# Kernel tuning notes

Measured on AMD Instinct MI355X. Metric: run time of the kernel, lower is better.

Reference implementation:

```python
import jax, jax.numpy as jnp
import numpy as np

B, C, E, H = 8, 2048, 1024, 128


def setup_inputs() -> dict:
    key = jax.random.key(0)
    k1, k2, k3, k4 = jax.random.split(key, 4)
    x = jax.random.normal(k1, (B, C, E), dtype=jnp.float32)
    # store projection weights as (E, H) so projection is x @ W
    Wq = jax.random.normal(k2, (E, H), dtype=jnp.float32) * (E ** -0.5)
    Wk = jax.random.normal(k3, (E, H), dtype=jnp.float32) * (E ** -0.5)
    Wv = jax.random.normal(k4, (E, H), dtype=jnp.float32) * (E ** -0.5)
    return {"x": x, "Wq": Wq, "Wk": Wk, "Wv": Wv}


def reference(x, Wq, Wk, Wv):
    # x: (B, C, E) -> out: (B, C, H)
    _, c, e = x.shape
    q = x @ Wq  # (B, C, H)
    k = x @ Wk  # (B, C, H)
    v = x @ Wv  # (B, C, H)
    # NOTE: original scales by embed_size**0.5, not head_size**0.5
    scale = jnp.asarray(e, x.dtype) ** 0.5
    w = jnp.einsum('bqh,bkh->bqk', q, k) / scale  # (B, C, C)
    causal = jnp.tril(jnp.ones((c, c), dtype=bool))
    w = jnp.where(causal, w, -jnp.inf)
    w = jax.nn.softmax(w, axis=-1)
    # dropout_rate = 0.0 -> identity (eval mode)
    out = w @ v  # (B, C, H)
    return out
```

## Files before the change

### kernel.cpp

```cpp
#include <hip/hip_runtime.h>
#include <hip/hip_bf16.h>
#include <stdint.h>

#define B_ 8
#define C_ 2048
#define E_ 1024
#define H_ 128
#define M_ (B_*C_)
#define SLOTS_B 144

typedef __attribute__((ext_vector_type(8))) short bf16x8;
typedef __attribute__((ext_vector_type(4))) float f32x4;

__device__ __forceinline__ unsigned short f2bf(float f) {
    union { float f; unsigned int u; } v; v.f = f;
    unsigned int u = v.u;
    u += 0x7fff + ((u >> 16) & 1);
    return (unsigned short)(u >> 16);
}
__device__ __forceinline__ float bf2f(unsigned short u) {
    union { unsigned int i; float f; } v; v.i = ((unsigned int)u) << 16; return v.f;
}

#define GLOAD_LDS16(g, l) \
    __builtin_amdgcn_global_load_lds((const __attribute__((address_space(1))) void*)(g), \
                                     (__attribute__((address_space(3))) void*)(l), 16, 0, 0)

__global__ __launch_bounds__(256) void wt2_kernel(const float* __restrict__ Wq,
                                                  const float* __restrict__ Wk,
                                                  const float* __restrict__ Wv,
                                                  unsigned short* __restrict__ WT2) {
    int z = blockIdx.y;
    const float* W = (z == 0) ? Wq : (z == 1) ? Wk : Wv;
    unsigned short* o = WT2 + (size_t)z * H_ * E_;
    int gid = blockIdx.x * 256 + threadIdx.x;
    int g = gid >> 7, h = gid & 127;
    unsigned short t[8];
#pragma unroll
    for (int j = 0; j < 8; ++j)
        t[j] = f2bf(W[(size_t)(g * 8 + j) * H_ + h]);
    *(bf16x8*)&o[(size_t)(g * 128 + h) * 8] = *(const bf16x8*)t;
}

#define MF(a, b, c) __builtin_amdgcn_mfma_f32_16x16x32_bf16((a), (b), (c), 0, 0, 0)

#define ALOAD(S, T) { const float* xs_ = xrow + (T) * 64; \
    a##S##_0 = *(const float4*)xs_;  a##S##_1 = *(const float4*)(xs_ + 4); }

#define AWRITE(S, BUF) { \
    unsigned short t_[8] = {f2bf(a##S##_0.x), f2bf(a##S##_0.y), f2bf(a##S##_0.z), f2bf(a##S##_0.w), \
                            f2bf(a##S##_1.x), f2bf(a##S##_1.y), f2bf(a##S##_1.z), f2bf(a##S##_1.w)}; \
    *(bf16x8*)&As[BUF][arow][(ag ^ (arow & 7)) * 8] = *(const bf16x8*)t_; }

#define COMPUTE(BUF, T) { \
    bf16x8 bw[3][2][2]; \
    _Pragma("unroll") for (int w_ = 0; w_ < 3; ++w_) \
    _Pragma("unroll") for (int ks_ = 0; ks_ < 2; ++ks_) \
    _Pragma("unroll") for (int ni_ = 0; ni_ < 2; ++ni_) \
        bw[w_][ni_][ks_] = *(const bf16x8*)&WT2[(size_t)w_ * H_ * E_ + \
            (size_t)(((T) * 8 + ks_ * 4 + lq) * 128 + wcol + ni_ * 16 + lrow) * 8]; \
    bf16x8 af[2][2]; \
    _Pragma("unroll") for (int mi_ = 0; mi_ < 2; ++mi_) \
    _Pragma("unroll") for (int ks_ = 0; ks_ < 2; ++ks_) { \
        int ra_ = mi_ * 16 + lrow; \
        af[mi_][ks_] = *(const bf16x8*)&As[BUF][ra_][((ks_ * 4 + lq) ^ (ra_ & 7)) * 8]; \
    } \
    _Pragma("unroll") for (int ks_ = 0; ks_ < 2; ++ks_) \
    _Pragma("unroll") for (int w_ = 0; w_ < 3; ++w_) \
    _Pragma("unroll") for (int ni_ = 0; ni_ < 2; ++ni_) \
    _Pragma("unroll") for (int mi_ = 0; mi_ < 2; ++mi_) \
        acc[w_][mi_][ni_] = MF(af[mi_][ks_], bw[w_][ni_][ks_], acc[w_][mi_][ni_]); }

#define EVEN_STEP(K) { \
    __syncthreads(); \
    if ((K) + 1 <= 15) AWRITE(B, 1);                \
    if ((K) + 2 <= 15) ALOAD(A, (K) + 2); \
    COMPUTE(0, K); }

#define ODD_STEP(K) { \
    __syncthreads(); \
    if ((K) + 1 <= 15) AWRITE(A, 0);                \
    if ((K) + 2 <= 15) ALOAD(B, (K) + 2); \
    COMPUTE(1, K); }

__global__ __launch_bounds__(256) void proj_kernel(const float* __restrict__ x,
                                                   const unsigned short* __restrict__ WT2,
                                                   unsigned short* __restrict__ QKV) {
    __shared__ __align__(16) unsigned short As[2][32][64];

    const int tid = threadIdx.x;
    const int wid = tid >> 6, lane = tid & 63;
    const int lrow = lane & 15, lq = lane >> 4;
    const int wcol = wid * 32;
    const int row0 = blockIdx.x * 32;

    const int arow = tid >> 3;
    const int ag = tid & 7;
    const float* xrow = x + (size_t)(row0 + arow) * E_ + ag * 8;

    f32x4 acc[3][2][2];
#pragma unroll
    for (int w = 0; w < 3; ++w)
#pragma unroll
        for (int mi = 0; mi < 2; ++mi)
#pragma unroll
            for (int ni = 0; ni < 2; ++ni) acc[w][mi][ni] = (f32x4){0.f, 0.f, 0.f, 0.f};

    float4 aA_0, aA_1, aB_0, aB_1;

    ALOAD(A, 0);
    AWRITE(A, 0);
    ALOAD(B, 1);

    EVEN_STEP(0)  ODD_STEP(1)  EVEN_STEP(2)  ODD_STEP(3)
    EVEN_STEP(4)  ODD_STEP(5)  EVEN_STEP(6)  ODD_STEP(7)
    EVEN_STEP(8)  ODD_STEP(9)  EVEN_STEP(10) ODD_STEP(11)
    EVEN_STEP(12) ODD_STEP(13) EVEN_STEP(14) ODD_STEP(15)

#pragma unroll
    for (int w = 0; w < 2; ++w) {
        const float qs = (w == 0) ? 0.03125f : 1.0f;
        unsigned short* outp = QKV + (size_t)w * M_ * H_;
#pragma unroll
        for (int mi = 0; mi < 2; ++mi) {
            int r0 = row0 + mi * 16 + lq * 4;
#pragma unroll
            for (int ni = 0; ni < 2; ++ni) {
                int col = wcol + ni * 16 + lrow;
#pragma unroll
                for (int r = 0; r < 4; ++r)
                    outp[(size_t)(r0 + r) * H_ + col] = f2bf(acc[w][mi][ni][r] * qs);
            }
        }
    }
    {
        unsigned short* vt = QKV + (size_t)2 * M_ * H_;
        int b = row0 / C_;
        int cbase = row0 % C_;
#pragma unroll
        for (int mi = 0; mi < 2; ++mi) {
            int c0 = cbase + mi * 16 + lq * 4;
#pragma unroll
            for (int ni = 0; ni < 2; ++ni) {
                int h = wcol + ni * 16 + lrow;
                __align__(8) unsigned short p[4] = {f2bf(acc[2][mi][ni][0]), f2bf(acc[2][mi][ni][1]),
                                                    f2bf(acc[2][mi][ni][2]), f2bf(acc[2][mi][ni][3])};
                *(uint2*)&vt[((size_t)b * H_ + h) * C_ + c0] = *(const uint2*)p;
            }
        }
    }
}

__global__ __launch_bounds__(256) void attn_kernel(const unsigned short* __restrict__ QKV,
                                                   unsigned short* __restrict__ PO,
                                                   float* __restrict__ ML,
                                                   float* __restrict__ out) {
    __shared__ __align__(16) unsigned short Ks[2][64][128];
    __shared__ __align__(16) unsigned short Vt[2][128][64];
    __shared__ __align__(16) unsigned short Ps[4][16][72];

    const unsigned short* Q  = QKV;
    const unsigned short* K  = QKV + (size_t)M_ * H_;
    const unsigned short* VT = QKV + (size_t)2 * M_ * H_;

    const int tid = threadIdx.x, wid = tid >> 6, lane = tid & 63;
    const int lrow = lane & 15, lq = lane >> 4, lk = lq * 8;
    const int rr = blockIdx.x;
    const int b = blockIdx.y;

    int j = 0;
#pragma unroll
    for (int jj = 1; jj < 32; ++jj) {
        int q = jj >> 2, s = jj & 3;
        if (jj + 2 * q * (q - 1) + s * q <= rr) j = jj;
    }
    const int qj = j >> 2, sj = j & 3;
    const int Cj = j + 2 * qj * (qj - 1) + sj * qj;
    const int c = rr - Cj;
    const int nch = qj + 1;
    const int t0 = c * 4;
    const int t1 = min(t0 + 4, j + 1);

    const int q0w = j * 64 + wid * 16;
    const unsigned short* Kb  = K  + (size_t)b * C_ * H_;
    const unsigned short* VTb = VT + (size_t)b * H_ * C_;
    const int qrow0 = q0w + lq * 4;

    const int krow = tid >> 4, kg = tid & 15;
    const int vrow = tid >> 3, vg = tid & 7;

    bf16x8 qf[4];
#pragma unroll
    for (int kf = 0; kf < 4; ++kf)
        qf[kf] = *(const bf16x8*)&Q[((size_t)b * C_ + q0w + lrow) * H_ + kf * 32 + lk];

    f32x4 o[8];
#pragma unroll
    for (int nf = 0; nf < 8; ++nf) o[nf] = (f32x4){0.f, 0.f, 0.f, 0.f};
    float m[4] = {-INFINITY, -INFINITY, -INFINITY, -INFINITY};
    float l[4] = {0.f, 0.f, 0.f, 0.f};

    auto STAGE = [&](int buf, int t) {
        const int kv0 = t * 64;
#pragma unroll
        for (int s = 0; s < 4; ++s) {
            int r = s * 16 + krow;
            GLOAD_LDS16(&Kb[(size_t)(kv0 + r) * H_ + ((kg ^ (r & 15)) * 8)],
                        (char*)&Ks[buf][0][0] + s * 4096 + tid * 16);
        }
#pragma unroll
        for (int s = 0; s < 4; ++s) {
            int h = s * 32 + vrow;
            GLOAD_LDS16(&VTb[(size_t)h * C_ + kv0 + ((vg ^ (h & 7)) * 8)],
                        (char*)&Vt[buf][0][0] + s * 4096 + tid * 16);
        }
    };

    STAGE(0, t0);

    for (int t = t0; t < t1; ++t) {
        const int cur = (t - t0) & 1;
        __syncthreads();
        if (t + 1 < t1) STAGE(cur ^ 1, t + 1);

        const int kv0 = t * 64;
        f32x4 s[4];
#pragma unroll
        for (int nf = 0; nf < 4; ++nf) {
            s[nf] = (f32x4){0.f, 0.f, 0.f, 0.f};
            const int rk = nf * 16 + lrow;
#pragma unroll
            for (int kf = 0; kf < 4; ++kf) {
                bf16x8 kb = *(const bf16x8*)&Ks[cur][rk][((kf * 4 + lq) ^ (rk & 15)) * 8];
                s[nf] = __builtin_amdgcn_mfma_f32_16x16x32_bf16(qf[kf], kb, s[nf], 0, 0, 0);
            }
        }
        bf16x8 vb[8][2];
#pragma unroll
        for (int nf = 0; nf < 8; ++nf) {
            const int h = nf * 16 + lrow;
#pragma unroll
            for (int kf2 = 0; kf2 < 2; ++kf2)
                vb[nf][kf2] = *(const bf16x8*)&Vt[cur][h][((kf2 * 4 + lq) ^ (h & 7)) * 8];
        }

        if (t == j) {
#pragma unroll
            for (int nf = 0; nf < 4; ++nf) {
                int key = kv0 + nf * 16 + lrow;
#pragma unroll
                for (int r = 0; r < 4; ++r)
                    if (key > qrow0 + r) s[nf][r] = -INFINITY;
            }
        }
        float mt[4] = {-INFINITY, -INFINITY, -INFINITY, -INFINITY};
#pragma unroll
        for (int nf = 0; nf < 4; ++nf)
#pragma unroll
            for (int r = 0; r < 4; ++r) mt[r] = fmaxf(mt[r], s[nf][r]);
#pragma unroll
        for (int r = 0; r < 4; ++r)
#pragma unroll
            for (int off = 1; off < 16; off <<= 1)
                mt[r] = fmaxf(mt[r], __shfl_xor(mt[r], off));

        float corr[4];
#pragma unroll
        for (int r = 0; r < 4; ++r) {
            float mn = fmaxf(m[r], mt[r]);
            corr[r] = __expf(m[r] - mn);
            m[r] = mn;
        }
        float ps[4] = {0.f, 0.f, 0.f, 0.f};
#pragma unroll
        for (int nf = 0; nf < 4; ++nf)
#pragma unroll
            for (int r = 0; r < 4; ++r) {
                float p = __expf(s[nf][r] - m[r]);
                ps[r] += p;
                Ps[wid][lq * 4 + r][nf * 16 + lrow] = f2bf(p);
            }
#pragma unroll
        for (int r = 0; r < 4; ++r) {
#pragma unroll
            for (int off = 1; off < 16; off <<= 1) ps[r] += __shfl_xor(ps[r], off);
            l[r] = l[r] * corr[r] + ps[r];
        }
#pragma unroll
        for (int nf = 0; nf < 8; ++nf)
#pragma unroll
            for (int r = 0; r < 4; ++r) o[nf][r] *= corr[r];

        bf16x8 pa[2];
#pragma unroll
        for (int kf2 = 0; kf2 < 2; ++kf2)
            pa[kf2] = *(const bf16x8*)&Ps[wid][lrow][kf2 * 32 + lk];
#pragma unroll
        for (int nf = 0; nf < 8; ++nf)
#pragma unroll
            for (int kf2 = 0; kf2 < 2; ++kf2)
                o[nf] = __builtin_amdgcn_mfma_f32_16x16x32_bf16(pa[kf2], vb[nf][kf2], o[nf], 0, 0, 0);
    }

    if (nch == 1) {
#pragma unroll
        for (int nf = 0; nf < 8; ++nf) {
            int col = nf * 16 + lrow;
#pragma unroll
            for (int r = 0; r < 4; ++r)
                out[((size_t)b * C_ + qrow0 + r) * H_ + col] = o[nf][r] / l[r];
        }
    } else {
        const int slot = b * SLOTS_B + rr;
        unsigned short* po = PO + (size_t)slot * 64 * 128;
        const int rl0 = wid * 16 + lq * 4;
#pragma unroll
        for (int nf = 0; nf < 8; ++nf) {
            int col = nf * 16 + lrow;
#pragma unroll
            for (int r = 0; r < 4; ++r)
                po[(size_t)(rl0 + r) * 128 + col] = f2bf(o[nf][r]);
        }
        if (lrow == 0) {
            float* ml = ML + (size_t)slot * 128;
#pragma unroll
            for (int r = 0; r < 4; ++r) {
                ml[rl0 + r] = m[r];
                ml[64 + rl0 + r] = l[r];
            }
        }
    }
}

__global__ __launch_bounds__(256) void combine_kernel(const unsigned short* __restrict__ PO,
                                                      const float* __restrict__ ML,
                                                      float* __restrict__ out) {
    const int j = blockIdx.x + 4;
    const int b = blockIdx.y;
    const int q = j >> 2, s = j & 3;
    const int Cj = j + 2 * q * (q - 1) + s * q;
    const int nch = q + 1;
    const int base = b * SLOTS_B + Cj;
    const int row = threadIdx.x >> 2;
    const int colg = (threadIdx.x & 3) * 32;

    float mstar = -INFINITY;
    for (int c = 0; c < nch; ++c)
        mstar = fmaxf(mstar, ML[(size_t)(base + c) * 128 + row]);

    float denom = 0.f;
    float acc[32];
#pragma unroll
    for (int i = 0; i < 32; ++i) acc[i] = 0.f;

    for (int c = 0; c < nch; ++c) {
        float mc = ML[(size_t)(base + c) * 128 + row];
        float lc = ML[(size_t)(base + c) * 128 + 64 + row];
        float w = __expf(mc - mstar);
        denom += w * lc;
        const unsigned short* p = PO + (size_t)(base + c) * 64 * 128 + (size_t)row * 128 + colg;
#pragma unroll
        for (int k = 0; k < 4; ++k) {
            bf16x8 v = *(const bf16x8*)&p[k * 8];
#pragma unroll
            for (int e = 0; e < 8; ++e)
                acc[k * 8 + e] += w * bf2f(((unsigned short*)&v)[e]);
        }
    }
    float inv = 1.f / denom;
    float* op = out + ((size_t)b * C_ + j * 64 + row) * H_ + colg;
#pragma unroll
    for (int k = 0; k < 8; ++k) {
        float4 st = {acc[k * 4] * inv, acc[k * 4 + 1] * inv, acc[k * 4 + 2] * inv, acc[k * 4 + 3] * inv};
        *(float4*)&op[k * 4] = st;
    }
}

extern "C" void kernel_launch(void* const* d_in, const int* in_sizes, int n_in,
                              void* d_out, int out_size, void* d_ws, size_t ws_size,
                              hipStream_t stream) {
    const float* x  = (const float*)d_in[0];
    const float* Wq = (const float*)d_in[1];
    const float* Wk = (const float*)d_in[2];
    const float* Wv = (const float*)d_in[3];
    float* out = (float*)d_out;

    unsigned short* WT2 = (unsigned short*)d_ws;
    unsigned short* QKV = WT2 + (size_t)3 * H_ * E_;
    unsigned short* PO  = QKV + (size_t)3 * M_ * H_;
    float*          ML  = (float*)(PO + (size_t)8 * SLOTS_B * 64 * 128);

    wt2_kernel<<<dim3(E_ / 8 * H_ / 256, 3), 256, 0, stream>>>(Wq, Wk, Wv, WT2);
    proj_kernel<<<dim3(M_ / 32), 256, 0, stream>>>(x, WT2, QKV);
    attn_kernel<<<dim3(SLOTS_B, B_), 256, 0, stream>>>(QKV, PO, ML, out);
    combine_kernel<<<dim3(28, B_), 256, 0, stream>>>(PO, ML, out);
}
```

Baseline: 79.46 us.

## Prefetch projection weights into registers, swap attention grid order, add MFMA priority

The projection kernel now prefetches the next K-step's weight fragments into a second register set while computing the current step, instead of loading weights from global memory right before the MFMAs. The A-tile write to shared memory moves after compute to overlap with it. The attention kernel swaps its grid axes so blocks with the same row-chunk index but different batches launch together, and wraps the MFMA sections in s_setprio to favour matrix issue. The register prefetch doubles the live weight fragments, which raises VGPR pressure and could reduce occupancy.

Result: faster. 76.27 us (-4.0%).

```diff
diff --git a/kernel.cpp b/kernel.cpp
--- a/kernel.cpp
+++ b/kernel.cpp
@@ -52,36 +52,41 @@
                             f2bf(a##S##_1.x), f2bf(a##S##_1.y), f2bf(a##S##_1.z), f2bf(a##S##_1.w)}; \
     *(bf16x8*)&As[BUF][arow][(ag ^ (arow & 7)) * 8] = *(const bf16x8*)t_; }
 
-#define COMPUTE(BUF, T) { \
-    bf16x8 bw[3][2][2]; \
-    _Pragma("unroll") for (int w_ = 0; w_ < 3; ++w_) \
-    _Pragma("unroll") for (int ks_ = 0; ks_ < 2; ++ks_) \
-    _Pragma("unroll") for (int ni_ = 0; ni_ < 2; ++ni_) \
-        bw[w_][ni_][ks_] = *(const bf16x8*)&WT2[(size_t)w_ * H_ * E_ + \
-            (size_t)(((T) * 8 + ks_ * 4 + lq) * 128 + wcol + ni_ * 16 + lrow) * 8]; \
-    bf16x8 af[2][2]; \
-    _Pragma("unroll") for (int mi_ = 0; mi_ < 2; ++mi_) \
-    _Pragma("unroll") for (int ks_ = 0; ks_ < 2; ++ks_) { \
-        int ra_ = mi_ * 16 + lrow; \
-        af[mi_][ks_] = *(const bf16x8*)&As[BUF][ra_][((ks_ * 4 + lq) ^ (ra_ & 7)) * 8]; \
-    } \
-    _Pragma("unroll") for (int ks_ = 0; ks_ < 2; ++ks_) \
-    _Pragma("unroll") for (int w_ = 0; w_ < 3; ++w_) \
-    _Pragma("unroll") for (int ni_ = 0; ni_ < 2; ++ni_) \
-    _Pragma("unroll") for (int mi_ = 0; mi_ < 2; ++mi_) \
-        acc[w_][mi_][ni_] = MF(af[mi_][ks_], bw[w_][ni_][ks_], acc[w_][mi_][ni_]); }
-
-#define EVEN_STEP(K) { \
-    __syncthreads(); \
-    if ((K) + 1 <= 15) AWRITE(B, 1);                \
-    if ((K) + 2 <= 15) ALOAD(A, (K) + 2); \
-    COMPUTE(0, K); }
-
-#define ODD_STEP(K) { \
-    __syncthreads(); \
-    if ((K) + 1 <= 15) AWRITE(A, 0);                \
-    if ((K) + 2 <= 15) ALOAD(B, (K) + 2); \
-    COMPUTE(1, K); }
+#define BLOAD(S, T) { const unsigned short* wp_ = wbase + (size_t)(T) * 8192; \
+    b##S##0  = *(const bf16x8*)(wp_);            b##S##1  = *(const bf16x8*)(wp_ + 128); \
+    b##S##2  = *(const bf16x8*)(wp_ + 4096);     b##S##3  = *(const bf16x8*)(wp_ + 4224); \
+    b##S##4  = *(const bf16x8*)(wp_ + 131072);   b##S##5  = *(const bf16x8*)(wp_ + 131200); \
+    b##S##6  = *(const bf16x8*)(wp_ + 135168);   b##S##7  = *(const bf16x8*)(wp_ + 135296); \
+    b##S##8  = *(const bf16x8*)(wp_ + 262144);   b##S##9  = *(const bf16x8*)(wp_ + 262272); \
+    b##S##10 = *(const bf16x8*)(wp_ + 266240);   b##S##11 = *(const bf16x8*)(wp_ + 266368); }
+
+#define COMPUTE(BUF, S) { \
+    bf16x8 af00 = *(const bf16x8*)&As[BUF][ra0][(lq ^ (ra0 & 7)) * 8]; \
+    bf16x8 af10 = *(const bf16x8*)&As[BUF][ra1][(lq ^ (ra1 & 7)) * 8]; \
+    acc[0][0][0] = MF(af00, b##S##0, acc[0][0][0]);  acc[0][1][0] = MF(af10, b##S##0, acc[0][1][0]); \
+    acc[0][0][1] = MF(af00, b##S##1, acc[0][0][1]);  acc[0][1][1] = MF(af10, b##S##1, acc[0][1][1]); \
+    acc[1][0][0] = MF(af00, b##S##4, acc[1][0][0]);  acc[1][1][0] = MF(af10, b##S##4, acc[1][1][0]); \
+    acc[1][0][1] = MF(af00, b##S##5, acc[1][0][1]);  acc[1][1][1] = MF(af10, b##S##5, acc[1][1][1]); \
+    acc[2][0][0] = MF(af00, b##S##8, acc[2][0][0]);  acc[2][1][0] = MF(af10, b##S##8, acc[2][1][0]); \
+    acc[2][0][1] = MF(af00, b##S##9, acc[2][0][1]);  acc[2][1][1] = MF(af10, b##S##9, acc[2][1][1]); \
+    bf16x8 af01 = *(const bf16x8*)&As[BUF][ra0][((4 + lq) ^ (ra0 & 7)) * 8]; \
+    bf16x8 af11 = *(const bf16x8*)&As[BUF][ra1][((4 + lq) ^ (ra1 & 7)) * 8]; \
+    acc[0][0][0] = MF(af01, b##S##2, acc[0][0][0]);  acc[0][1][0] = MF(af11, b##S##2, acc[0][1][0]); \
+    acc[0][0][1] = MF(af01, b##S##3, acc[0][0][1]);  acc[0][1][1] = MF(af11, b##S##3, acc[0][1][1]); \
+    acc[1][0][0] = MF(af01, b##S##6, acc[1][0][0]);  acc[1][1][0] = MF(af11, b##S##6, acc[1][1][0]); \
+    acc[1][0][1] = MF(af01, b##S##7, acc[1][0][1]);  acc[1][1][1] = MF(af11, b##S##7, acc[1][1][1]); \
+    acc[2][0][0] = MF(af01, b##S##10, acc[2][0][0]); acc[2][1][0] = MF(af11, b##S##10, acc[2][1][0]); \
+    acc[2][0][1] = MF(af01, b##S##11, acc[2][0][1]); acc[2][1][1] = MF(af11, b##S##11, acc[2][1][1]); }
+
+#define STEP_E(K) { __syncthreads(); \
+    if ((K) < 15) { ALOAD(O, (K)+1); BLOAD(O, (K)+1); } \
+    COMPUTE((K)&1, E); \
+    if ((K) < 15) AWRITE(O, ((K)+1)&1); }
+
+#define STEP_O(K) { __syncthreads(); \
+    if ((K) < 15) { ALOAD(E, (K)+1); BLOAD(E, (K)+1); } \
+    COMPUTE((K)&1, O); \
+    if ((K) < 15) AWRITE(E, ((K)+1)&1); }
 
 __global__ __launch_bounds__(256) void proj_kernel(const float* __restrict__ x,
                                                    const unsigned short* __restrict__ WT2,
@@ -97,6 +102,8 @@
     const int arow = tid >> 3;
     const int ag = tid & 7;
     const float* xrow = x + (size_t)(row0 + arow) * E_ + ag * 8;
+    const int ra0 = lrow, ra1 = 16 + lrow;
+    const unsigned short* wbase = WT2 + (size_t)(lq * 128 + wcol + lrow) * 8;
 
     f32x4 acc[3][2][2];
 #pragma unroll
@@ -106,16 +113,17 @@
 #pragma unroll
             for (int ni = 0; ni < 2; ++ni) acc[w][mi][ni] = (f32x4){0.f, 0.f, 0.f, 0.f};
 
-    float4 aA_0, aA_1, aB_0, aB_1;
-
-    ALOAD(A, 0);
-    AWRITE(A, 0);
-    ALOAD(B, 1);
-
-    EVEN_STEP(0)  ODD_STEP(1)  EVEN_STEP(2)  ODD_STEP(3)
-    EVEN_STEP(4)  ODD_STEP(5)  EVEN_STEP(6)  ODD_STEP(7)
-    EVEN_STEP(8)  ODD_STEP(9)  EVEN_STEP(10) ODD_STEP(11)
-    EVEN_STEP(12) ODD_STEP(13) EVEN_STEP(14) ODD_STEP(15)
+    float4 aE_0, aE_1, aO_0, aO_1;
+    bf16x8 bE0, bE1, bE2, bE3, bE4, bE5, bE6, bE7, bE8, bE9, bE10, bE11;
+    bf16x8 bO0, bO1, bO2, bO3, bO4, bO5, bO6, bO7, bO8, bO9, bO10, bO11;
+
+    ALOAD(E, 0); BLOAD(E, 0);
+    AWRITE(E, 0);
+
+    STEP_E(0)  STEP_O(1)  STEP_E(2)  STEP_O(3)
+    STEP_E(4)  STEP_O(5)  STEP_E(6)  STEP_O(7)
+    STEP_E(8)  STEP_O(9)  STEP_E(10) STEP_O(11)
+    STEP_E(12) STEP_O(13) STEP_E(14) STEP_O(15)
 
 #pragma unroll
     for (int w = 0; w < 2; ++w) {
@@ -165,8 +173,8 @@
 
     const int tid = threadIdx.x, wid = tid >> 6, lane = tid & 63;
     const int lrow = lane & 15, lq = lane >> 4, lk = lq * 8;
-    const int rr = blockIdx.x;
-    const int b = blockIdx.y;
+    const int b = blockIdx.x;
+    const int rr = blockIdx.y;
 
     int j = 0;
 #pragma unroll
@@ -225,6 +233,7 @@
 
         const int kv0 = t * 64;
         f32x4 s[4];
+        __builtin_amdgcn_s_setprio(1);
 #pragma unroll
         for (int nf = 0; nf < 4; ++nf) {
             s[nf] = (f32x4){0.f, 0.f, 0.f, 0.f};
@@ -235,6 +244,7 @@
                 s[nf] = __builtin_amdgcn_mfma_f32_16x16x32_bf16(qf[kf], kb, s[nf], 0, 0, 0);
             }
         }
+        __builtin_amdgcn_s_setprio(0);
         bf16x8 vb[8][2];
 #pragma unroll
         for (int nf = 0; nf < 8; ++nf) {
@@ -295,11 +305,13 @@
 #pragma unroll
         for (int kf2 = 0; kf2 < 2; ++kf2)
             pa[kf2] = *(const bf16x8*)&Ps[wid][lrow][kf2 * 32 + lk];
+        __builtin_amdgcn_s_setprio(1);
 #pragma unroll
         for (int nf = 0; nf < 8; ++nf)
 #pragma unroll
             for (int kf2 = 0; kf2 < 2; ++kf2)
                 o[nf] = __builtin_amdgcn_mfma_f32_16x16x32_bf16(pa[kf2], vb[nf][kf2], o[nf], 0, 0, 0);
+        __builtin_amdgcn_s_setprio(0);
     }
 
     if (nch == 1) {
@@ -392,6 +404,6 @@
 
     wt2_kernel<<<dim3(E_ / 8 * H_ / 256, 3), 256, 0, stream>>>(Wq, Wk, Wv, WT2);
     proj_kernel<<<dim3(M_ / 32), 256, 0, stream>>>(x, WT2, QKV);
-    attn_kernel<<<dim3(SLOTS_B, B_), 256, 0, stream>>>(QKV, PO, ML, out);
+    attn_kernel<<<dim3(B_, SLOTS_B), 256, 0, stream>>>(QKV, PO, ML, out);
     combine_kernel<<<dim3(28, B_), 256, 0, stream>>>(PO, ML, out);
 }
```
